# Kernel optimization log

Measured on AMD Instinct MI355X. Metric: run time of the kernel, lower is better.

Reference implementation:

```python
import jax, jax.numpy as jnp
import numpy as np

# config matching init_kwargs: stox_params=[4,2,1,1,64,2], in=64, out=128, k=3, pad=1
A_BITS = 4          # a_slices = a_bits / a_bits_per_stream = 4
W_SLICES = 2        # w_bits / w_bits_per_slice = 2
NUM_CHUNKS = 9      # ceil(64*9/64)
SUB = 64            # crossbar chunk width
ITERS = 2           # stochastic iterations
EPS = 1e-5          # BatchNorm1d eps


def ste(y, x):
    # straight-through estimator: forward y, backward identity of x
    return x + jax.lax.stop_gradient(y - x)


def unfold3x3(x):
    # torch F.unfold(x, 3, dilation=1, padding=1, stride=1): [B,C,H,W] -> [B, C*9, H*W]
    B, C, H, W = x.shape
    xp = jnp.pad(x, ((0, 0), (0, 0), (1, 1), (1, 1)))
    cols = [xp[:, :, i:i + H, j:j + W] for i in range(3) for j in range(3)]
    return jnp.stack(cols, axis=2).reshape(B, C * 9, H * W)  # (c, kh, kw) ordering


def setup_inputs() -> dict:
    key = jax.random.key(0)
    k1, k2 = jax.random.split(key)
    inputs = jax.random.normal(k1, (8, 64, 32, 32), jnp.float32)
    fan_in = 64 * 9  # kaiming_normal_ fan_in
    weight = jax.random.normal(k2, (128 * W_SLICES, 64, 3, 3), jnp.float32) * np.float32(np.sqrt(2.0 / fan_in))
    bn_gamma = jnp.ones((128 * W_SLICES,), jnp.float32)
    bn_beta = jnp.zeros((128 * W_SLICES,), jnp.float32)
    return {"inputs": inputs, "weight": weight, "bn_gamma": bn_gamma, "bn_beta": bn_beta}


def reference(inputs, weight, bn_gamma, bn_beta):
    O = weight.shape[0]  # out_channels * W_SLICES = 256
    # --- per-output-row weight standardization + 1-bit STE quantization (WeightQuantize) ---
    wf = weight.reshape(O, -1)                       # [O, Cin*9]
    bw = wf - wf.mean(-1, keepdims=True)
    bw = bw / bw.std(-1, ddof=1, keepdims=True)      # torch std is unbiased
    qw = ste(jnp.sign(bw), bw)                       # [O, Cin*9]
    # --- unfold + multi-bit input stream (create_input_stream): bit-planes stacked on batch dim ---
    a = unfold3x3(inputs)                            # [B, Cin*9, L]
    Bsz, C9, L = a.shape
    x = jnp.clip(a, 0.0, 1.0)
    q = jnp.round(x * (2 ** A_BITS - 1))
    bits = jnp.stack([jnp.floor(q / (2 ** i)) % 2 for i in range(A_BITS)], 0)  # [A,B,C9,L]
    qa = bits.reshape(A_BITS * Bsz, C9, L)
    # --- chunked crossbar linear + BatchNorm1d(train) + MTJ sign, summed over chunks/iterations ---
    out = jnp.zeros((A_BITS * Bsz, O, L), a.dtype)
    for c in range(NUM_CHUNKS):
        wk = qa[:, c * SUB:(c + 1) * SUB, :]         # [B', SUB, L]
        ww = qw[:, c * SUB:(c + 1) * SUB]            # [O, SUB]
        for _ in range(ITERS):
            lin = jnp.einsum('bcl,oc->bol', wk, ww)  # [B', O, L]
            mu = lin.mean((0, 2), keepdims=True)
            var = lin.var((0, 2), keepdims=True)     # biased, as torch BN training
            bn = bn_gamma[None, :, None] * (lin - mu) / jnp.sqrt(var + EPS) + bn_beta[None, :, None]
            out = out + ste(jnp.sign(bn), bn)        # MTJ stochastic comparator -> sign w/ STE
    # --- bit-weighted reconstructions ---
    wvec = (2.0 ** jnp.arange(W_SLICES, dtype=a.dtype)) / (2 ** W_SLICES - 1)
    out = jnp.einsum('s,bsol->bol', wvec, out.reshape(A_BITS * Bsz, W_SLICES, O // W_SLICES, L))
    avec = (2.0 ** jnp.arange(A_BITS, dtype=a.dtype)) / (2 ** A_BITS - 1)
    out = jnp.einsum('a,abol->bol', avec, out.reshape(A_BITS, Bsz, O // W_SLICES, L))
    # --- F.fold with (1,1) kernel == reshape to square spatial map ---
    P = int(np.sqrt(L))
    return out.reshape(Bsz, O // W_SLICES, P, P)
```

## Files before the change

kernel.cpp:

```cpp
#include <hip/hip_runtime.h>
#include <cstdint>
#include <cstddef>

static const size_t OFF_ACT  = 0;
static const size_t OFF_W    = OFF_ACT + 2359296;
static const size_t OFF_T    = OFF_W   + 18432;
static const size_t OFF_NS1  = OFF_T   + 18432;
static const size_t OFF_MUG  = OFF_NS1 + 9216;
static const size_t OFF_FLAG = OFF_MUG + 18432;
static const size_t OFF_WB   = OFF_FLAG + 1024;

typedef int v4i __attribute__((ext_vector_type(4)));

__device__ __forceinline__ int isgn(int e) {
  int t = e < -1 ? -1 : e;
  return t > 1 ? 1 : t;
}

__global__ __launch_bounds__(256) void k_prep(const float* __restrict__ x,
                                              const float* __restrict__ w,
                                              const float* __restrict__ gamma,
                                              const float* __restrict__ beta,
                                              int* __restrict__ T,
                                              uint64_t* __restrict__ act,
                                              uint64_t* __restrict__ wbits,
                                              int* __restrict__ flag,
                                              signed char* __restrict__ wbyte) {
  int bid = blockIdx.x;
  int tid = threadIdx.x;
  if (bid < 512) {
    int base = bid << 10;
    int vals[9];
#pragma unroll
    for (int k = 0; k < 9; ++k) vals[k] = 0;
#pragma unroll
    for (int i = 0; i < 4; ++i) {
      int px = tid + i * 256;
      int h = px >> 5, ww = px & 31;
      float v = x[base + px];
      v = fminf(fmaxf(v, 0.f), 1.f);
      int q = (int)rintf(v * 15.f);
      int pc = __popc((unsigned)q);
      vals[0] += pc;
      if (h == 0) vals[1] += pc;
      if (h == 31) vals[2] += pc;
      if (ww == 0) vals[3] += pc;
      if (ww == 31) vals[4] += pc;
      if (h == 0 && ww == 0) vals[5] += pc;
      if (h == 0 && ww == 31) vals[6] += pc;
      if (h == 31 && ww == 0) vals[7] += pc;
      if (h == 31 && ww == 31) vals[8] += pc;
    }
#pragma unroll
    for (int k = 0; k < 9; ++k)
      for (int off = 32; off; off >>= 1) vals[k] += __shfl_down(vals[k], off, 64);
    __shared__ int red[4][9];
    int wid = tid >> 6, lane = tid & 63;
    if (lane == 0)
#pragma unroll
      for (int k = 0; k < 9; ++k) red[wid][k] = vals[k];
    __syncthreads();
    if (tid < 9) T[bid * 9 + tid] = red[0][tid] + red[1][tid] + red[2][tid] + red[3][tid];
  } else if (bid < 1664) {
    int gidx = (bid - 512) * 256 + tid;
    int half = gidx & 3;
    int idx = gidx >> 2;
    int l = idx & 1023;
    int c = (idx >> 10) % 9;
    int b = idx / (9 * 1024);
    int h = l >> 5, w0 = l & 31;
    int i9 = c * 64 + half * 16;
    int ch = i9 / 9;
    int k = i9 - ch * 9;
    int ki = k / 3, kj = k - ki * 3;
    unsigned m0 = 0, m1 = 0, m2 = 0, m3 = 0;
#pragma unroll
    for (int jj = 0; jj < 16; ++jj) {
      int hh = h + ki - 1, ww = w0 + kj - 1;
      int q = 0;
      if ((unsigned)hh < 32u && (unsigned)ww < 32u) {
        float v = x[(((b * 64 + ch) << 10) + (hh << 5)) + ww];
        v = fminf(fmaxf(v, 0.f), 1.f);
        q = (int)rintf(v * 15.f);
      }
      m0 |= (unsigned)(q & 1) << jj;
      m1 |= (unsigned)((q >> 1) & 1) << jj;
      m2 |= (unsigned)((q >> 2) & 1) << jj;
      m3 |= (unsigned)((q >> 3) & 1) << jj;
      if (++kj == 3) { kj = 0; if (++ki == 3) { ki = 0; ++ch; } }
    }
    size_t stride = 8 * 9 * 1024;
    size_t off = ((size_t)b * 9 + c) * 1024 + l;
    unsigned short* a16 = (unsigned short*)act;
    a16[(0 * stride + off) * 4 + half] = (unsigned short)m0;
    a16[(1 * stride + off) * 4 + half] = (unsigned short)m1;
    a16[(2 * stride + off) * 4 + half] = (unsigned short)m2;
    a16[(3 * stride + off) * 4 + half] = (unsigned short)m3;
  } else {
    int lane = tid & 63;
    int wid = tid >> 6;
    int o = (bid - 1664) * 4 + wid;
    const float* row = w + (size_t)o * 576;
    double s = 0.0;
#pragma unroll
    for (int i = 0; i < 9; ++i) s += (double)row[lane + i * 64];
    for (int off = 32; off; off >>= 1) s += __shfl_down(s, off, 64);
    s = __shfl(s, 0, 64);
    float mean = (float)(s / 576.0);
#pragma unroll
    for (int c = 0; c < 9; ++c) {
      float v = row[c * 64 + lane];
      int pos = (v - mean) > 0.f;
      unsigned long long m = __ballot(pos);
      if (lane == 0) wbits[o * 9 + c] = (uint64_t)m;
      wbyte[(c * 256 + o) * 64 + lane] = pos ? (signed char)1 : (signed char)-1;
    }
    if (lane == 0) flag[o] = (beta[o] == 0.f && gamma[o] > 0.f) ? 1 : 0;
  }
}

__global__ __launch_bounds__(256) void k_s1(const int* __restrict__ T,
                                            const uint64_t* __restrict__ wbits,
                                            const int* __restrict__ flag,
                                            const float* __restrict__ gamma,
                                            const uint64_t* __restrict__ act,
                                            int* __restrict__ negS1,
                                            float2* __restrict__ MUG) {
  __shared__ int Tsh[576];
  __shared__ int Ush[9 * 65];
  int tid = threadIdx.x;
  for (int i = tid; i < 576; i += 256) {
    int acc = 0;
#pragma unroll
    for (int b = 0; b < 8; ++b) acc += T[b * 576 + i];
    Tsh[i] = acc;
  }
  __syncthreads();
  for (int i = tid; i < 576; i += 256) {
    int ch = i / 9;
    int k = i - ch * 9;
    int ki = k / 3, kj = k - ki * 3;
    const int* t = &Tsh[ch * 9];
    int u = t[0];
    if (ki == 0) u -= t[2]; else if (ki == 2) u -= t[1];
    if (kj == 0) u -= t[4]; else if (kj == 2) u -= t[3];
    if (ki == 0 && kj == 0) u += t[8];
    if (ki == 0 && kj == 2) u += t[7];
    if (ki == 2 && kj == 0) u += t[6];
    if (ki == 2 && kj == 2) u += t[5];
    Ush[(i >> 6) * 65 + (i & 63)] = u;
  }
  __syncthreads();
  int pair = blockIdx.x * 256 + tid;
  int o = pair / 9, c = pair - o * 9;
  uint64_t wv = wbits[pair];
  int tot = 0, pos = 0;
#pragma unroll 8
  for (int j = 0; j < 64; ++j) {
    int cnt = Ush[c * 65 + j];
    tot += cnt;
    if ((wv >> j) & 1) pos += cnt;
  }
  int s1 = 2 * pos - tot;
  negS1[c * 256 + o] = -s1;
  if (!flag[o]) {
    int s2 = 0;
    for (int i = 0; i < 32768; ++i) {
      uint64_t av = act[((size_t)(i >> 10) * 9 + c) * 1024 + (i & 1023)];
      int lin = 2 * __popcll(av & wv) - __popcll(av);
      s2 += lin * lin;
    }
    float mu = (float)s1 * (1.f / 32768.f);
    float ex2 = (float)s2 * (1.f / 32768.f);
    float var = ex2 - mu * mu;
    if (var < 0.f) var = 0.f;
    MUG[pair] = make_float2(mu, gamma[o] / sqrtf(var + 1e-5f));
  }
}

__global__ __launch_bounds__(256, 2) void k_out(const uint64_t* __restrict__ act,
                                                const signed char* __restrict__ wbyte,
                                                const int* __restrict__ negS1g,
                                                const float2* __restrict__ MUG,
                                                const int* __restrict__ flag,
                                                const float* __restrict__ beta,
                                                float* __restrict__ out) {
  __shared__ int nsh[2304];
  int tid = threadIdx.x;
  int lt = blockIdx.x;
  int b = blockIdx.y;
  for (int i = tid; i < 2304; i += 256) nsh[i] = negS1g[i];
  __syncthreads();

  int lane = tid & 63;
  int w = __builtin_amdgcn_readfirstlane(tid >> 6);
  int row = lane & 15;
  int g = lane >> 4;

  int o0 = w * 32 + (lane & 31);
  int fb = flag[o0] & flag[o0 + 128];
  bool fastAll = (bool)__all(fb != 0);

  const v4i zacc = {0, 0, 0, 0};
  int l = lt * 16 + row;

  if (fastAll) {
    int M[2][4] = {{0, 0, 0, 0}, {0, 0, 0, 0}};
    for (int c = 0; c < 9; ++c) {
      v4i Af[4];
      int nS[4][4];
#pragma unroll
      for (int q = 0; q < 4; ++q) {
        int ot = 2 * w + (q & 1) + (q >> 1) * 8;
        Af[q] = *(const v4i*)(wbyte + ((size_t)(c * 256 + ot * 16 + row) * 64 + g * 16));
#pragma unroll
        for (int r = 0; r < 4; ++r) nS[q][r] = nsh[c * 256 + ot * 16 + g * 4 + r];
      }
#pragma unroll
      for (int a = 0; a < 4; ++a) {
        size_t idx = ((size_t)(a * 8 + b) * 9 + c) * 1024 + l;
        unsigned dw = *(const unsigned*)((const char*)act + idx * 8 + (g >> 1) * 4);
        unsigned bits = (dw >> ((g & 1) * 16)) & 0xFFFFu;
        v4i Bf;
#pragma unroll
        for (int d = 0; d < 4; ++d)
          Bf[d] = (int)((((bits >> (4 * d)) & 0xFu) * 0x00204081u) & 0x01010101u);
#pragma unroll
        for (int q = 0; q < 4; ++q) {
          v4i acc = __builtin_amdgcn_mfma_i32_16x16x64_i8(Af[q], Bf, zacc, 0, 0, 0);
#pragma unroll
          for (int r = 0; r < 4; ++r) {
            int e = (acc[r] << 15) + nS[q][r];
            M[q & 1][r] += isgn(e) << (a + (q >> 1));
          }
        }
      }
    }
#pragma unroll
    for (int q2 = 0; q2 < 2; ++q2)
#pragma unroll
      for (int r = 0; r < 4; ++r) {
        int oo = (2 * w + q2) * 16 + g * 4 + r;
        out[((size_t)b * 128 + oo) * 1024 + l] = (float)M[q2][r] * (2.f / 45.f);
      }
  } else {
    int M[2][4] = {{0, 0, 0, 0}, {0, 0, 0, 0}};
    float F[2][4] = {{0.f, 0.f, 0.f, 0.f}, {0.f, 0.f, 0.f, 0.f}};
    int flv[4][4];
#pragma unroll
    for (int q = 0; q < 4; ++q) {
      int ot = 2 * w + (q & 1) + (q >> 1) * 8;
#pragma unroll
      for (int r = 0; r < 4; ++r) flv[q][r] = flag[ot * 16 + g * 4 + r];
    }
    for (int c = 0; c < 9; ++c) {
      v4i Af[4];
      int nS[4][4];
#pragma unroll
      for (int q = 0; q < 4; ++q) {
        int ot = 2 * w + (q & 1) + (q >> 1) * 8;
        Af[q] = *(const v4i*)(wbyte + ((size_t)(c * 256 + ot * 16 + row) * 64 + g * 16));
#pragma unroll
        for (int r = 0; r < 4; ++r) nS[q][r] = nsh[c * 256 + ot * 16 + g * 4 + r];
      }
#pragma unroll
      for (int a = 0; a < 4; ++a) {
        size_t idx = ((size_t)(a * 8 + b) * 9 + c) * 1024 + l;
        unsigned dw = *(const unsigned*)((const char*)act + idx * 8 + (g >> 1) * 4);
        unsigned bits = (dw >> ((g & 1) * 16)) & 0xFFFFu;
        v4i Bf;
#pragma unroll
        for (int d = 0; d < 4; ++d)
          Bf[d] = (int)((((bits >> (4 * d)) & 0xFu) * 0x00204081u) & 0x01010101u);
#pragma unroll
        for (int q = 0; q < 4; ++q) {
          v4i acc = __builtin_amdgcn_mfma_i32_16x16x64_i8(Af[q], Bf, zacc, 0, 0, 0);
          int ot = 2 * w + (q & 1) + (q >> 1) * 8;
#pragma unroll
          for (int r = 0; r < 4; ++r) {
            int lin = acc[r];
            if (flv[q][r]) {
              M[q & 1][r] += isgn((lin << 15) + nS[q][r]) << (a + (q >> 1));
            } else {
              int o = ot * 16 + g * 4 + r;
              float2 m2 = MUG[o * 9 + c];
              float bn = m2.y * ((float)lin - m2.x) + beta[o];
              float sg = (bn > 0.f) ? 1.f : ((bn < 0.f) ? -1.f : 0.f);
              F[q & 1][r] += sg * (float)(1 << (a + (q >> 1)));
            }
          }
        }
      }
    }
#pragma unroll
    for (int q2 = 0; q2 < 2; ++q2)
#pragma unroll
      for (int r = 0; r < 4; ++r) {
        int oo = (2 * w + q2) * 16 + g * 4 + r;
        out[((size_t)b * 128 + oo) * 1024 + l] =
            ((float)M[q2][r] + F[q2][r]) * (2.f / 45.f);
      }
  }
}

extern "C" void kernel_launch(void* const* d_in, const int* in_sizes, int n_in,
                              void* d_out, int out_size, void* d_ws, size_t ws_size,
                              hipStream_t stream) {
  const float* inputs = (const float*)d_in[0];
  const float* weight = (const float*)d_in[1];
  const float* gamma = (const float*)d_in[2];
  const float* beta = (const float*)d_in[3];
  float* out = (float*)d_out;

  char* ws = (char*)d_ws;
  uint64_t* act = (uint64_t*)(ws + OFF_ACT);
  uint64_t* wbits = (uint64_t*)(ws + OFF_W);
  int* T = (int*)(ws + OFF_T);
  int* negS1 = (int*)(ws + OFF_NS1);
  float2* MUG = (float2*)(ws + OFF_MUG);
  int* flag = (int*)(ws + OFF_FLAG);
  signed char* wbyte = (signed char*)(ws + OFF_WB);

  k_prep<<<1728, 256, 0, stream>>>(inputs, weight, gamma, beta, T, act, wbits, flag, wbyte);
  k_s1<<<9, 256, 0, stream>>>(T, wbits, flag, gamma, act, negS1, MUG);
  k_out<<<dim3(64, 8), 256, 0, stream>>>(act, wbyte, negS1, MUG, flag, beta, out);
}
```

Baseline: 95.39 us.

## Split k_out output channels across two block groups to raise occupancy

Each wave of k_out now handles one output tile pair (t, t+8) instead of two pairs. The grid doubles along a new output-group dimension, and launch bounds are raised to 4 blocks per SM. Activation bit-planes for all four streams are loaded up front, before the MFMAs run. This gives more waves and fewer registers per wave to hide memory latency, at the cost of loading the activations twice and repeating the shared-memory fill of negS1 in twice as many blocks.

```diff
diff --git a/kernel.cpp b/kernel.cpp
--- a/kernel.cpp
+++ b/kernel.cpp
@@ -178,7 +178,7 @@
   }
 }
 
-__global__ __launch_bounds__(256, 2) void k_out(const uint64_t* __restrict__ act,
+__global__ __launch_bounds__(256, 4) void k_out(const uint64_t* __restrict__ act,
                                                 const signed char* __restrict__ wbyte,
                                                 const int* __restrict__ negS1g,
                                                 const float2* __restrict__ MUG,
@@ -188,118 +188,123 @@
   __shared__ int nsh[2304];
   int tid = threadIdx.x;
   int lt = blockIdx.x;
-  int b = blockIdx.y;
+  int og = blockIdx.y;
+  int b = blockIdx.z;
   for (int i = tid; i < 2304; i += 256) nsh[i] = negS1g[i];
   __syncthreads();
 
   int lane = tid & 63;
   int w = __builtin_amdgcn_readfirstlane(tid >> 6);
+  int t = og * 4 + w;
   int row = lane & 15;
   int g = lane >> 4;
 
-  int o0 = w * 32 + (lane & 31);
-  int fb = flag[o0] & flag[o0 + 128];
+  int fb = flag[t * 16 + row] & flag[(t + 8) * 16 + row];
   bool fastAll = (bool)__all(fb != 0);
 
   const v4i zacc = {0, 0, 0, 0};
   int l = lt * 16 + row;
 
   if (fastAll) {
-    int M[2][4] = {{0, 0, 0, 0}, {0, 0, 0, 0}};
+    int M0[4] = {0, 0, 0, 0}, M1[4] = {0, 0, 0, 0};
     for (int c = 0; c < 9; ++c) {
-      v4i Af[4];
-      int nS[4][4];
-#pragma unroll
-      for (int q = 0; q < 4; ++q) {
-        int ot = 2 * w + (q & 1) + (q >> 1) * 8;
-        Af[q] = *(const v4i*)(wbyte + ((size_t)(c * 256 + ot * 16 + row) * 64 + g * 16));
-#pragma unroll
-        for (int r = 0; r < 4; ++r) nS[q][r] = nsh[c * 256 + ot * 16 + g * 4 + r];
-      }
+      v4i Af0 = *(const v4i*)(wbyte + ((size_t)(c * 256 + t * 16 + row) * 64 + g * 16));
+      v4i Af1 = *(const v4i*)(wbyte + ((size_t)(c * 256 + (t + 8) * 16 + row) * 64 + g * 16));
+      int nS0[4], nS1[4];
+#pragma unroll
+      for (int r = 0; r < 4; ++r) {
+        nS0[r] = nsh[c * 256 + t * 16 + g * 4 + r];
+        nS1[r] = nsh[c * 256 + (t + 8) * 16 + g * 4 + r];
+      }
+      unsigned bits[4];
 #pragma unroll
       for (int a = 0; a < 4; ++a) {
         size_t idx = ((size_t)(a * 8 + b) * 9 + c) * 1024 + l;
         unsigned dw = *(const unsigned*)((const char*)act + idx * 8 + (g >> 1) * 4);
-        unsigned bits = (dw >> ((g & 1) * 16)) & 0xFFFFu;
+        bits[a] = (dw >> ((g & 1) * 16)) & 0xFFFFu;
+      }
+#pragma unroll
+      for (int a = 0; a < 4; ++a) {
         v4i Bf;
 #pragma unroll
         for (int d = 0; d < 4; ++d)
-          Bf[d] = (int)((((bits >> (4 * d)) & 0xFu) * 0x00204081u) & 0x01010101u);
-#pragma unroll
-        for (int q = 0; q < 4; ++q) {
-          v4i acc = __builtin_amdgcn_mfma_i32_16x16x64_i8(Af[q], Bf, zacc, 0, 0, 0);
-#pragma unroll
-          for (int r = 0; r < 4; ++r) {
-            int e = (acc[r] << 15) + nS[q][r];
-            M[q & 1][r] += isgn(e) << (a + (q >> 1));
-          }
+          Bf[d] = (int)((((bits[a] >> (4 * d)) & 0xFu) * 0x00204081u) & 0x01010101u);
+        v4i acc0 = __builtin_amdgcn_mfma_i32_16x16x64_i8(Af0, Bf, zacc, 0, 0, 0);
+        v4i acc1 = __builtin_amdgcn_mfma_i32_16x16x64_i8(Af1, Bf, zacc, 0, 0, 0);
+#pragma unroll
+        for (int r = 0; r < 4; ++r) {
+          M0[r] += isgn((acc0[r] << 15) + nS0[r]) << a;
+          M1[r] += isgn((acc1[r] << 15) + nS1[r]) << (a + 1);
         }
       }
     }
 #pragma unroll
-    for (int q2 = 0; q2 < 2; ++q2)
+    for (int r = 0; r < 4; ++r) {
+      int oo = t * 16 + g * 4 + r;
+      out[((size_t)b * 128 + oo) * 1024 + l] = (float)(M0[r] + M1[r]) * (2.f / 45.f);
+    }
+  } else {
+    int M0[4] = {0, 0, 0, 0}, M1[4] = {0, 0, 0, 0};
+    float F[4] = {0.f, 0.f, 0.f, 0.f};
+    int fl0[4], fl1[4];
+#pragma unroll
+    for (int r = 0; r < 4; ++r) {
+      fl0[r] = flag[t * 16 + g * 4 + r];
+      fl1[r] = flag[(t + 8) * 16 + g * 4 + r];
+    }
+    for (int c = 0; c < 9; ++c) {
+      v4i Af0 = *(const v4i*)(wbyte + ((size_t)(c * 256 + t * 16 + row) * 64 + g * 16));
+      v4i Af1 = *(const v4i*)(wbyte + ((size_t)(c * 256 + (t + 8) * 16 + row) * 64 + g * 16));
+      int nS0[4], nS1[4];
 #pragma unroll
       for (int r = 0; r < 4; ++r) {
-        int oo = (2 * w + q2) * 16 + g * 4 + r;
-        out[((size_t)b * 128 + oo) * 1024 + l] = (float)M[q2][r] * (2.f / 45.f);
-      }
-  } else {
-    int M[2][4] = {{0, 0, 0, 0}, {0, 0, 0, 0}};
-    float F[2][4] = {{0.f, 0.f, 0.f, 0.f}, {0.f, 0.f, 0.f, 0.f}};
-    int flv[4][4];
-#pragma unroll
-    for (int q = 0; q < 4; ++q) {
-      int ot = 2 * w + (q & 1) + (q >> 1) * 8;
-#pragma unroll
-      for (int r = 0; r < 4; ++r) flv[q][r] = flag[ot * 16 + g * 4 + r];
-    }
-    for (int c = 0; c < 9; ++c) {
-      v4i Af[4];
-      int nS[4][4];
-#pragma unroll
-      for (int q = 0; q < 4; ++q) {
-        int ot = 2 * w + (q & 1) + (q >> 1) * 8;
-        Af[q] = *(const v4i*)(wbyte + ((size_t)(c * 256 + ot * 16 + row) * 64 + g * 16));
-#pragma unroll
-        for (int r = 0; r < 4; ++r) nS[q][r] = nsh[c * 256 + ot * 16 + g * 4 + r];
-      }
+        nS0[r] = nsh[c * 256 + t * 16 + g * 4 + r];
+        nS1[r] = nsh[c * 256 + (t + 8) * 16 + g * 4 + r];
+      }
+      unsigned bits[4];
 #pragma unroll
       for (int a = 0; a < 4; ++a) {
         size_t idx = ((size_t)(a * 8 + b) * 9 + c) * 1024 + l;
         unsigned dw = *(const unsigned*)((const char*)act + idx * 8 + (g >> 1) * 4);
-        unsigned bits = (dw >> ((g & 1) * 16)) & 0xFFFFu;
+        bits[a] = (dw >> ((g & 1) * 16)) & 0xFFFFu;
+      }
+#pragma unroll
+      for (int a = 0; a < 4; ++a) {
         v4i Bf;
 #pragma unroll
         for (int d = 0; d < 4; ++d)
-          Bf[d] = (int)((((bits >> (4 * d)) & 0xFu) * 0x00204081u) & 0x01010101u);
-#pragma unroll
-        for (int q = 0; q < 4; ++q) {
-          v4i acc = __builtin_amdgcn_mfma_i32_16x16x64_i8(Af[q], Bf, zacc, 0, 0, 0);
-          int ot = 2 * w + (q & 1) + (q >> 1) * 8;
-#pragma unroll
-          for (int r = 0; r < 4; ++r) {
-            int lin = acc[r];
-            if (flv[q][r]) {
-              M[q & 1][r] += isgn((lin << 15) + nS[q][r]) << (a + (q >> 1));
-            } else {
-              int o = ot * 16 + g * 4 + r;
-              float2 m2 = MUG[o * 9 + c];
-              float bn = m2.y * ((float)lin - m2.x) + beta[o];
-              float sg = (bn > 0.f) ? 1.f : ((bn < 0.f) ? -1.f : 0.f);
-              F[q & 1][r] += sg * (float)(1 << (a + (q >> 1)));
-            }
+          Bf[d] = (int)((((bits[a] >> (4 * d)) & 0xFu) * 0x00204081u) & 0x01010101u);
+        v4i acc0 = __builtin_amdgcn_mfma_i32_16x16x64_i8(Af0, Bf, zacc, 0, 0, 0);
+        v4i acc1 = __builtin_amdgcn_mfma_i32_16x16x64_i8(Af1, Bf, zacc, 0, 0, 0);
+#pragma unroll
+        for (int r = 0; r < 4; ++r) {
+          if (fl0[r]) {
+            M0[r] += isgn((acc0[r] << 15) + nS0[r]) << a;
+          } else {
+            int o = t * 16 + g * 4 + r;
+            float2 m2 = MUG[o * 9 + c];
+            float bn = m2.y * ((float)acc0[r] - m2.x) + beta[o];
+            float sg = (bn > 0.f) ? 1.f : ((bn < 0.f) ? -1.f : 0.f);
+            F[r] += sg * (float)(1 << a);
+          }
+          if (fl1[r]) {
+            M1[r] += isgn((acc1[r] << 15) + nS1[r]) << (a + 1);
+          } else {
+            int o = (t + 8) * 16 + g * 4 + r;
+            float2 m2 = MUG[o * 9 + c];
+            float bn = m2.y * ((float)acc1[r] - m2.x) + beta[o];
+            float sg = (bn > 0.f) ? 1.f : ((bn < 0.f) ? -1.f : 0.f);
+            F[r] += sg * (float)(1 << (a + 1));
           }
         }
       }
     }
 #pragma unroll
-    for (int q2 = 0; q2 < 2; ++q2)
-#pragma unroll
-      for (int r = 0; r < 4; ++r) {
-        int oo = (2 * w + q2) * 16 + g * 4 + r;
-        out[((size_t)b * 128 + oo) * 1024 + l] =
-            ((float)M[q2][r] + F[q2][r]) * (2.f / 45.f);
-      }
+    for (int r = 0; r < 4; ++r) {
+      int oo = t * 16 + g * 4 + r;
+      out[((size_t)b * 128 + oo) * 1024 + l] =
+          ((float)(M0[r] + M1[r]) + F[r]) * (2.f / 45.f);
+    }
   }
 }
 
@@ -323,5 +328,5 @@
 
   k_prep<<<1728, 256, 0, stream>>>(inputs, weight, gamma, beta, T, act, wbits, flag, wbyte);
   k_s1<<<9, 256, 0, stream>>>(T, wbits, flag, gamma, act, negS1, MUG);
-  k_out<<<dim3(64, 8), 256, 0, stream>>>(act, wbyte, negS1, MUG, flag, beta, out);
-}
+  k_out<<<dim3(64, 2, 8), 256, 0, stream>>>(act, wbyte, negS1, MUG, flag, beta, out);
+}
```

New measurement: 96.37 us. Within noise of the previous version (+1.0%).
